# Performance work log

Measured on AMD Instinct MI355X. Metric: run time of the kernel, lower is better.

Reference implementation:

```python
import jax, jax.numpy as jnp
import numpy as np

NP, NA, E, DIN, DOUT = 50000, 50000, 800000, 128, 128


def setup_inputs() -> dict:
    key = jax.random.key(0)
    ks = jax.random.split(key, 16)
    inp = {
        'h_paper': jax.random.normal(ks[0], (NP, DIN), jnp.float32),
        'h_author': jax.random.normal(ks[1], (NA, DIN), jnp.float32),
        'W_r1': jax.random.normal(ks[2], (DIN, DOUT), jnp.float32) / np.sqrt(DIN),
        'W_r2': jax.random.normal(ks[3], (DIN, DOUT), jnp.float32) / np.sqrt(DIN),
        'W_r3': jax.random.normal(ks[4], (DIN, DOUT), jnp.float32) / np.sqrt(DIN),
        'att_W': jax.random.normal(ks[5], (DOUT, 128), jnp.float32) / np.sqrt(DOUT),
        'att_b': jax.random.normal(ks[6], (128,), jnp.float32) * 0.02,
        'att_q': jax.random.normal(ks[7], (128,), jnp.float32) / np.sqrt(128.0),
        'bn_gamma': jnp.ones((DOUT,), jnp.float32),
        'bn_beta': jnp.zeros((DOUT,), jnp.float32),
        'src_r1': jax.random.randint(ks[8], (E,), 0, NA, jnp.int32),
        'dst_r1': jax.random.randint(ks[9], (E,), 0, NP, jnp.int32),
        'src_r2': jax.random.randint(ks[10], (E,), 0, NP, jnp.int32),
        'dst_r2': jax.random.randint(ks[11], (E,), 0, NP, jnp.int32),
        'src_r3': jax.random.randint(ks[12], (E,), 0, NA, jnp.int32),
        'dst_r3': jax.random.randint(ks[13], (E,), 0, NA, jnp.int32),
    }
    return inp


def _graph_conv(h_src, W, src, dst, n_src, n_dst):
    # DGL GraphConv, norm='both', bias=False
    ones = jnp.ones(src.shape[0], h_src.dtype)
    deg_out = jnp.clip(jax.ops.segment_sum(ones, src, num_segments=n_src), 1.0)
    deg_in = jnp.clip(jax.ops.segment_sum(ones, dst, num_segments=n_dst), 1.0)
    m = (h_src * jax.lax.rsqrt(deg_out)[:, None]) @ W          # [n_src, Dout]
    agg = jax.ops.segment_sum(m[src], dst, num_segments=n_dst)  # [n_dst, Dout]
    return agg * jax.lax.rsqrt(deg_in)[:, None]


def _semantic_attention(z, att_W, att_b, att_q):
    # z: [R, N, D] per-relation outputs for one destination node type
    w = jnp.mean(jnp.tanh(z @ att_W + att_b) @ att_q, axis=1)  # [R]
    beta = jax.nn.softmax(w)
    return jnp.einsum('r,rnd->nd', beta, z)


def _post(x, gamma, beta):
    mu = jnp.mean(x, axis=0)
    var = jnp.var(x, axis=0)
    x = (x - mu) * jax.lax.rsqrt(var + 1e-5) * gamma + beta  # BatchNorm1d (train stats)
    return x * jax.lax.rsqrt(jnp.sum(x * x, axis=-1, keepdims=True) + 1e-12)  # L2 norm


def reference(h_paper, h_author, W_r1, W_r2, W_r3, att_W, att_b, att_q,
              bn_gamma, bn_beta, src_r1, dst_r1, src_r2, dst_r2, src_r3, dst_r3):
    n_p, n_a = h_paper.shape[0], h_author.shape[0]
    z_p1 = _graph_conv(h_author, W_r1, src_r1, dst_r1, n_a, n_p)  # author->paper
    z_p2 = _graph_conv(h_paper, W_r2, src_r2, dst_r2, n_p, n_p)   # paper->paper
    z_a1 = _graph_conv(h_author, W_r3, src_r3, dst_r3, n_a, n_a)  # author->author
    out_p = _semantic_attention(jnp.stack([z_p1, z_p2]), att_W, att_b, att_q)
    out_a = _semantic_attention(z_a1[None], att_W, att_b, att_q)
    out_p = _post(out_p, bn_gamma, bn_beta)
    out_a = _post(out_a, bn_gamma, bn_beta)
    return out_p, out_a
```

## Files before the change

kernel.cpp:

```cpp
#include <hip/hip_runtime.h>

#define DIM 128
#define NBLK 64
#define MAXTB 2560

static inline size_t align256(size_t x) { return (x + 255) & ~(size_t)255; }

__global__ void k_dout(const int* __restrict__ s1, int E1,
                       const int* __restrict__ s2, int E2,
                       const int* __restrict__ s3, int E3,
                       int* __restrict__ dout, int NM) {
  int i = blockIdx.x * blockDim.x + threadIdx.x;
  int st = gridDim.x * blockDim.x;
  int ET = E1 + E2 + E3;
  for (; i < ET; i += st) {
    const int* sp; int j, r;
    if (i < E1) { r = 0; j = i; sp = s1; }
    else if (i < E1 + E2) { r = 1; j = i - E1; sp = s2; }
    else { r = 2; j = i - E1 - E2; sp = s3; }
    atomicAdd(&dout[r * NM + sp[j]], 1);
  }
}

__global__ __launch_bounds__(256) void k_hist(const int* __restrict__ d1, int E1,
                                              const int* __restrict__ d2, int E2,
                                              const int* __restrict__ d3, int E3,
                                              int* __restrict__ Hmat, int NB, int TB) {
  __shared__ int hl[MAXTB];
  int t = threadIdx.x, b = blockIdx.x;
  for (int k = t; k < TB; k += 256) hl[k] = 0;
  __syncthreads();
  int ET = E1 + E2 + E3;
  int CH = (ET + NBLK - 1) / NBLK;
  int lo = b * CH, hi = min(lo + CH, ET);
  for (int i = lo + t; i < hi; i += 256) {
    const int* dp; int j, r;
    if (i < E1) { r = 0; j = i; dp = d1; }
    else if (i < E1 + E2) { r = 1; j = i - E1; dp = d2; }
    else { r = 2; j = i - E1 - E2; dp = d3; }
    int kb = r * NB + (dp[j] >> 6);
    atomicAdd(&hl[kb], 1);
  }
  __syncthreads();
  for (int k = t; k < TB; k += 256) Hmat[(size_t)k * NBLK + b] = hl[k];
}

__global__ __launch_bounds__(256) void k_scan1(const int* __restrict__ cnt,
                                               int* __restrict__ part, int M) {
  __shared__ int wsh[4];
  int t = threadIdx.x;
  int base = blockIdx.x * 2048 + t * 8;
  int s = 0;
  if (base + 8 <= M) {
    const int4* p = (const int4*)(cnt + base);
    int4 a = p[0], b = p[1];
    s = a.x + a.y + a.z + a.w + b.x + b.y + b.z + b.w;
  } else {
    for (int j = 0; j < 8; ++j) { int idx = base + j; if (idx < M) s += cnt[idx]; }
  }
#pragma unroll
  for (int off = 32; off; off >>= 1) s += __shfl_down(s, off, 64);
  int lane = t & 63, wid = t >> 6;
  if (lane == 0) wsh[wid] = s;
  __syncthreads();
  if (t == 0) part[blockIdx.x] = wsh[0] + wsh[1] + wsh[2] + wsh[3];
}

__global__ __launch_bounds__(256) void k_scan2(int* __restrict__ part, int B,
                                               int* __restrict__ rp, int M) {
  __shared__ int sh[256];
  int t = threadIdx.x;
  sh[t] = (t < B) ? part[t] : 0;
  __syncthreads();
  for (int off = 1; off < 256; off <<= 1) {
    int v = (t >= off) ? sh[t - off] : 0;
    __syncthreads();
    sh[t] += v;
    __syncthreads();
  }
  if (t < B) part[t] = t ? sh[t - 1] : 0;
  if (t == 0) rp[M] = sh[255];
}

__global__ __launch_bounds__(256) void k_scan3(const int* __restrict__ cnt,
                                               const int* __restrict__ part,
                                               int* __restrict__ rp, int M) {
  __shared__ int wsh[4];
  int t = threadIdx.x, lane = t & 63, wid = t >> 6;
  int base = blockIdx.x * 2048 + t * 8;
  int v[8];
  if (base + 8 <= M) {
    const int4* p = (const int4*)(cnt + base);
    int4 a = p[0], b = p[1];
    v[0] = a.x; v[1] = a.y; v[2] = a.z; v[3] = a.w;
    v[4] = b.x; v[5] = b.y; v[6] = b.z; v[7] = b.w;
  } else {
    for (int j = 0; j < 8; ++j) { int idx = base + j; v[j] = (idx < M) ? cnt[idx] : 0; }
  }
  int ts = 0;
#pragma unroll
  for (int j = 0; j < 8; ++j) ts += v[j];
  int incl = ts;
#pragma unroll
  for (int d = 1; d < 64; d <<= 1) { int u = __shfl_up(incl, d, 64); if (lane >= d) incl += u; }
  if (lane == 63) wsh[wid] = incl;
  __syncthreads();
  int woff = 0;
  for (int w = 0; w < wid; ++w) woff += wsh[w];
  int run = part[blockIdx.x] + woff + incl - ts;
#pragma unroll
  for (int j = 0; j < 8; ++j) {
    int idx = base + j;
    if (idx < M) rp[idx] = run;
    run += v[j];
  }
}

__global__ __launch_bounds__(256) void k_scatter(const int* __restrict__ s1, const int* __restrict__ d1, int E1,
                                                 const int* __restrict__ s2, const int* __restrict__ d2, int E2,
                                                 const int* __restrict__ s3, const int* __restrict__ d3, int E3,
                                                 const int* __restrict__ rp,
                                                 unsigned* __restrict__ ebuf, int NB, int TB) {
  __shared__ int curl[MAXTB];
  int t = threadIdx.x, b = blockIdx.x;
  for (int k = t; k < TB; k += 256) curl[k] = rp[(size_t)k * NBLK + b];
  __syncthreads();
  int ET = E1 + E2 + E3;
  int CH = (ET + NBLK - 1) / NBLK;
  int lo = b * CH, hi = min(lo + CH, ET);
  for (int i = lo + t; i < hi; i += 256) {
    const int* sp; const int* dp; int j, r;
    if (i < E1) { r = 0; j = i; sp = s1; dp = d1; }
    else if (i < E1 + E2) { r = 1; j = i - E1; sp = s2; dp = d2; }
    else { r = 2; j = i - E1 - E2; sp = s3; dp = d3; }
    int dst = dp[j];
    int kb = r * NB + (dst >> 6);
    int pos = atomicAdd(&curl[kb], 1);
    ebuf[pos] = ((unsigned)(dst & 63) << 16) | (unsigned)sp[j];
  }
}

__global__ __launch_bounds__(256) void k_bsort(const unsigned* __restrict__ ebuf,
                                               const int* __restrict__ rp,
                                               unsigned short* __restrict__ ebuf2,
                                               int* __restrict__ rp2, int* __restrict__ deg,
                                               int NB, int NM) {
  __shared__ int hist[64];
  __shared__ int cursor[64];
  int t = threadIdx.x;
  int k = blockIdx.x;
  if (t < 64) hist[t] = 0;
  __syncthreads();
  int start = rp[(size_t)k * NBLK];
  int end = rp[(size_t)(k + 1) * NBLK];
  for (int e = start + t; e < end; e += 256)
    atomicAdd(&hist[ebuf[e] >> 16], 1);
  __syncthreads();
  if (t < 64) {
    int v = hist[t];
    int incl = v;
#pragma unroll
    for (int d = 1; d < 64; d <<= 1) { int u = __shfl_up(incl, d, 64); if (t >= d) incl += u; }
    int excl = incl - v;
    cursor[t] = start + excl;
    int r = k / NB, bb = k - r * NB;
    int ld = bb * 64 + t;
    if (ld < NM) {
      rp2[r * NM + ld] = start + excl;
      deg[r * NM + ld] = v;
    }
  }
  __syncthreads();
  for (int e = start + t; e < end; e += 256) {
    unsigned p = ebuf[e];
    int pos = atomicAdd(&cursor[p >> 16], 1);
    ebuf2[pos] = (unsigned short)(p & 0xFFFF);
  }
}

__global__ __launch_bounds__(256) void k_pull2(const float* __restrict__ m,
                                               const int* __restrict__ rp2,
                                               const int* __restrict__ deg,
                                               const unsigned short* __restrict__ ebuf2,
                                               float* __restrict__ z, int N) {
  int lane = threadIdx.x & 63, wid = threadIdx.x >> 6;
  int gw = blockIdx.x * 4 + wid, nw = gridDim.x * 4;
  for (int n = gw; n < N; n += nw) {
    int b = rp2[n], d = deg[n];
    float ax = 0.f, ay = 0.f;
    for (int e = b; e < b + d; ++e) {
      int s = ebuf2[e];
      float2 v = *(const float2*)(m + (size_t)s * DIM + 2 * lane);
      ax += v.x; ay += v.y;
    }
    float sc = rsqrtf(fmaxf((float)d, 1.0f));
    float2 o; o.x = ax * sc; o.y = ay * sc;
    *(float2*)(z + (size_t)n * DIM + 2 * lane) = o;
  }
}

__global__ __launch_bounds__(512) void k_gemm(const float* __restrict__ h,
                                              const float* __restrict__ W,
                                              const int* __restrict__ degout,
                                              float* __restrict__ m, int N) {
  __shared__ float Wl[DIM * DIM];
  for (int i = threadIdx.x; i < DIM * DIM; i += 512) Wl[i] = W[i];
  __syncthreads();
  int lane = threadIdx.x & 63, wid = threadIdx.x >> 6;
  int gw = blockIdx.x * 8 + wid, nw = gridDim.x * 8;
  for (int n = gw; n < N; n += nw) {
    float s = rsqrtf(fmaxf((float)degout[n], 1.0f));
    const float4* h4 = (const float4*)(h + (size_t)n * DIM);
    float ax = 0.f, ay = 0.f;
#pragma unroll 4
    for (int k4 = 0; k4 < 32; ++k4) {
      float4 hv = h4[k4];
      int k = k4 * 4;
      float2 w0 = *(const float2*)&Wl[(k + 0) * DIM + 2 * lane];
      float2 w1 = *(const float2*)&Wl[(k + 1) * DIM + 2 * lane];
      float2 w2 = *(const float2*)&Wl[(k + 2) * DIM + 2 * lane];
      float2 w3 = *(const float2*)&Wl[(k + 3) * DIM + 2 * lane];
      ax = fmaf(hv.x, w0.x, ax); ay = fmaf(hv.x, w0.y, ay);
      ax = fmaf(hv.y, w1.x, ax); ay = fmaf(hv.y, w1.y, ay);
      ax = fmaf(hv.z, w2.x, ax); ay = fmaf(hv.z, w2.y, ay);
      ax = fmaf(hv.w, w3.x, ax); ay = fmaf(hv.w, w3.y, ay);
    }
    float2 o; o.x = s * ax; o.y = s * ay;
    *(float2*)(m + (size_t)n * DIM + 2 * lane) = o;
  }
}

__global__ __launch_bounds__(512) void k_att(const float* __restrict__ z1,
                                             const float* __restrict__ z2,
                                             const float* __restrict__ attW,
                                             const float* __restrict__ attb,
                                             const float* __restrict__ attq,
                                             float* __restrict__ wsum, int N) {
  __shared__ float Wl[DIM * DIM];
  for (int i = threadIdx.x; i < DIM * DIM; i += 512) Wl[i] = attW[i];
  int lane = threadIdx.x & 63, wid = threadIdx.x >> 6;
  float b0 = attb[2 * lane], b1 = attb[2 * lane + 1];
  float q0 = attq[2 * lane], q1 = attq[2 * lane + 1];
  __syncthreads();
  int gw = blockIdx.x * 8 + wid, nw = gridDim.x * 8;
  float a1 = 0.f, a2 = 0.f;
  for (int n = gw; n < N; n += nw) {
    const float4* p1 = (const float4*)(z1 + (size_t)n * DIM);
    const float4* p2 = (const float4*)(z2 + (size_t)n * DIM);
    float c1x = 0, c1y = 0, c2x = 0, c2y = 0;
#pragma unroll 4
    for (int k4 = 0; k4 < 32; ++k4) {
      float4 u = p1[k4];
      float4 v = p2[k4];
      int k = k4 * 4;
      float2 w0 = *(const float2*)&Wl[(k + 0) * DIM + 2 * lane];
      float2 w1 = *(const float2*)&Wl[(k + 1) * DIM + 2 * lane];
      float2 w2 = *(const float2*)&Wl[(k + 2) * DIM + 2 * lane];
      float2 w3 = *(const float2*)&Wl[(k + 3) * DIM + 2 * lane];
      c1x = fmaf(u.x, w0.x, c1x); c1y = fmaf(u.x, w0.y, c1y);
      c2x = fmaf(v.x, w0.x, c2x); c2y = fmaf(v.x, w0.y, c2y);
      c1x = fmaf(u.y, w1.x, c1x); c1y = fmaf(u.y, w1.y, c1y);
      c2x = fmaf(v.y, w1.x, c2x); c2y = fmaf(v.y, w1.y, c2y);
      c1x = fmaf(u.z, w2.x, c1x); c1y = fmaf(u.z, w2.y, c1y);
      c2x = fmaf(v.z, w2.x, c2x); c2y = fmaf(v.z, w2.y, c2y);
      c1x = fmaf(u.w, w3.x, c1x); c1y = fmaf(u.w, w3.y, c1y);
      c2x = fmaf(v.w, w3.x, c2x); c2y = fmaf(v.w, w3.y, c2y);
    }
    a1 += tanhf(c1x + b0) * q0 + tanhf(c1y + b1) * q1;
    a2 += tanhf(c2x + b0) * q0 + tanhf(c2y + b1) * q1;
  }
#pragma unroll
  for (int off = 32; off; off >>= 1) {
    a1 += __shfl_down(a1, off, 64);
    a2 += __shfl_down(a2, off, 64);
  }
  __syncthreads();
  if (lane == 0) { Wl[wid] = a1; Wl[8 + wid] = a2; }
  __syncthreads();
  if (threadIdx.x == 0) {
    float s1 = 0, s2 = 0;
    for (int w = 0; w < 8; ++w) { s1 += Wl[w]; s2 += Wl[8 + w]; }
    atomicAdd(&wsum[0], s1);
    atomicAdd(&wsum[1], s2);
  }
}

__global__ void k_combine(float* __restrict__ x, const float* __restrict__ z2,
                          const float* __restrict__ wsum, float invN, int total4) {
  float w1 = wsum[0] * invN, w2 = wsum[1] * invN;
  float mx = fmaxf(w1, w2);
  float e1 = expf(w1 - mx), e2 = expf(w2 - mx);
  float inv = 1.f / (e1 + e2);
  float b1 = e1 * inv, b2 = e2 * inv;
  float4* x4 = (float4*)x;
  const float4* z4 = (const float4*)z2;
  int i = blockIdx.x * blockDim.x + threadIdx.x;
  int st = gridDim.x * blockDim.x;
  for (; i < total4; i += st) {
    float4 a = x4[i], b = z4[i];
    a.x = b1 * a.x + b2 * b.x;
    a.y = b1 * a.y + b2 * b.y;
    a.z = b1 * a.z + b2 * b.z;
    a.w = b1 * a.w + b2 * b.w;
    x4[i] = a;
  }
}

__global__ __launch_bounds__(128) void k_stats2(const float* __restrict__ xp,
                                                const float* __restrict__ xa,
                                                int NP, int NA, float* __restrict__ st) {
  int d = threadIdx.x;
  float sp = 0, qp = 0, sa = 0, qa = 0;
  for (int n = blockIdx.x; n < NP; n += gridDim.x) {
    float v = xp[(size_t)n * DIM + d]; sp += v; qp += v * v;
  }
  for (int n = blockIdx.x; n < NA; n += gridDim.x) {
    float v = xa[(size_t)n * DIM + d]; sa += v; qa += v * v;
  }
  atomicAdd(&st[d], sp);
  atomicAdd(&st[DIM + d], qp);
  atomicAdd(&st[2 * DIM + d], sa);
  atomicAdd(&st[3 * DIM + d], qa);
}

__global__ __launch_bounds__(256) void k_post2(float* __restrict__ xp, float* __restrict__ xa,
                                               const float* __restrict__ st,
                                               const float* __restrict__ gamma,
                                               const float* __restrict__ beta,
                                               int NP, int NA) {
  int lane = threadIdx.x & 63;
  int wv = blockIdx.x * 4 + (threadIdx.x >> 6), nw = gridDim.x * 4;
  int d0 = 2 * lane, d1 = d0 + 1;
  {
    float invN = 1.f / (float)NP;
    float mu0 = st[d0] * invN, mu1 = st[d1] * invN;
    float g0 = gamma[d0] * rsqrtf(st[DIM + d0] * invN - mu0 * mu0 + 1e-5f);
    float g1 = gamma[d1] * rsqrtf(st[DIM + d1] * invN - mu1 * mu1 + 1e-5f);
    float b0 = beta[d0], b1 = beta[d1];
    for (int n = wv; n < NP; n += nw) {
      float2 v = *(float2*)(xp + (size_t)n * DIM + d0);
      float y0 = fmaf(v.x - mu0, g0, b0);
      float y1 = fmaf(v.y - mu1, g1, b1);
      float p = y0 * y0 + y1 * y1;
#pragma unroll
      for (int off = 32; off; off >>= 1) p += __shfl_xor(p, off, 64);
      float r = rsqrtf(p + 1e-12f);
      float2 o; o.x = y0 * r; o.y = y1 * r;
      *(float2*)(xp + (size_t)n * DIM + d0) = o;
    }
  }
  {
    float invN = 1.f / (float)NA;
    float mu0 = st[2 * DIM + d0] * invN, mu1 = st[2 * DIM + d1] * invN;
    float g0 = gamma[d0] * rsqrtf(st[3 * DIM + d0] * invN - mu0 * mu0 + 1e-5f);
    float g1 = gamma[d1] * rsqrtf(st[3 * DIM + d1] * invN - mu1 * mu1 + 1e-5f);
    float b0 = beta[d0], b1 = beta[d1];
    for (int n = wv; n < NA; n += nw) {
      float2 v = *(float2*)(xa + (size_t)n * DIM + d0);
      float y0 = fmaf(v.x - mu0, g0, b0);
      float y1 = fmaf(v.y - mu1, g1, b1);
      float p = y0 * y0 + y1 * y1;
#pragma unroll
      for (int off = 32; off; off >>= 1) p += __shfl_xor(p, off, 64);
      float r = rsqrtf(p + 1e-12f);
      float2 o; o.x = y0 * r; o.y = y1 * r;
      *(float2*)(xa + (size_t)n * DIM + d0) = o;
    }
  }
}

extern "C" void kernel_launch(void* const* d_in, const int* in_sizes, int n_in,
                              void* d_out, int out_size, void* d_ws, size_t ws_size,
                              hipStream_t stream) {
  const float* h_paper  = (const float*)d_in[0];
  const float* h_author = (const float*)d_in[1];
  const float* W_r1 = (const float*)d_in[2];
  const float* W_r2 = (const float*)d_in[3];
  const float* W_r3 = (const float*)d_in[4];
  const float* att_W = (const float*)d_in[5];
  const float* att_b = (const float*)d_in[6];
  const float* att_q = (const float*)d_in[7];
  const float* bn_g = (const float*)d_in[8];
  const float* bn_b = (const float*)d_in[9];
  const int* src_r1 = (const int*)d_in[10];
  const int* dst_r1 = (const int*)d_in[11];
  const int* src_r2 = (const int*)d_in[12];
  const int* dst_r2 = (const int*)d_in[13];
  const int* src_r3 = (const int*)d_in[14];
  const int* dst_r3 = (const int*)d_in[15];

  int NP = in_sizes[0] / DIM;
  int NA = in_sizes[1] / DIM;
  int E1 = in_sizes[10], E2 = in_sizes[12], E3 = in_sizes[14];
  int ET = E1 + E2 + E3;
  int NM = NP > NA ? NP : NA;
  int NB = (NM + 63) >> 6;
  int TB = 3 * NB;
  int M = TB * NBLK;
  int B = (M + 2047) / 2048;

  char* ws = (char*)d_ws;
  size_t off = 0;
  float* m_buf = (float*)(ws + off);    off += align256((size_t)NM * DIM * 4);
  float* z2    = (float*)(ws + off);    off += align256((size_t)NP * DIM * 4);
  unsigned* ebuf = (unsigned*)(ws + off); off += align256((size_t)ET * 4);
  unsigned short* ebuf2 = (unsigned short*)(ws + off); off += align256((size_t)ET * 2);
  int* Hmat    = (int*)(ws + off);      off += align256((size_t)M * 4);
  int* rp      = (int*)(ws + off);      off += align256(((size_t)M + 1) * 4);
  int* rp2     = (int*)(ws + off);      off += align256((size_t)3 * NM * 4);
  int* deg     = (int*)(ws + off);      off += align256((size_t)3 * NM * 4);
  int* part    = (int*)(ws + off);      off += align256(256 * 4);
  size_t zoff = off;
  int* dout    = (int*)(ws + off);      off += (size_t)3 * NM * 4;
  float* wsum  = (float*)(ws + off);    off += 2 * 4;
  float* stats = (float*)(ws + off);    off += 4 * DIM * 4;
  size_t zbytes = off - zoff;

  float* xp = (float*)d_out;
  float* xa = (float*)d_out + (size_t)NP * DIM;

  hipMemsetAsync(ws + zoff, 0, zbytes, stream);

  k_dout<<<2048, 256, 0, stream>>>(src_r1, E1, src_r2, E2, src_r3, E3, dout, NM);

  k_hist<<<NBLK, 256, 0, stream>>>(dst_r1, E1, dst_r2, E2, dst_r3, E3, Hmat, NB, TB);
  k_scan1<<<B, 256, 0, stream>>>(Hmat, part, M);
  k_scan2<<<1, 256, 0, stream>>>(part, B, rp, M);
  k_scan3<<<B, 256, 0, stream>>>(Hmat, part, rp, M);
  k_scatter<<<NBLK, 256, 0, stream>>>(src_r1, dst_r1, E1, src_r2, dst_r2, E2,
                                      src_r3, dst_r3, E3, rp, ebuf, NB, TB);
  k_bsort<<<TB, 256, 0, stream>>>(ebuf, rp, ebuf2, rp2, deg, NB, NM);

  k_gemm<<<512, 512, 0, stream>>>(h_author, W_r1, dout, m_buf, NA);
  k_pull2<<<2048, 256, 0, stream>>>(m_buf, rp2, deg, ebuf2, xp, NP);
  k_gemm<<<512, 512, 0, stream>>>(h_paper, W_r2, dout + NM, m_buf, NP);
  k_pull2<<<2048, 256, 0, stream>>>(m_buf, rp2 + NM, deg + NM, ebuf2, z2, NP);
  k_gemm<<<512, 512, 0, stream>>>(h_author, W_r3, dout + 2 * NM, m_buf, NA);
  k_pull2<<<2048, 256, 0, stream>>>(m_buf, rp2 + 2 * NM, deg + 2 * NM, ebuf2, xa, NA);

  k_att<<<512, 512, 0, stream>>>(xp, z2, att_W, att_b, att_q, wsum, NP);
  k_combine<<<2048, 256, 0, stream>>>(xp, z2, wsum, 1.0f / (float)NP, NP * DIM / 4);

  k_stats2<<<1024, 128, 0, stream>>>(xp, xa, NP, NA, stats);
  k_post2<<<2048, 256, 0, stream>>>(xp, xa, stats, bn_g, bn_b, NP, NA);
}
```

Baseline: 1.015 ms.

## Register-block GEMM and attention over four nodes, split pull wavefront into halves

The GEMM and attention kernels now process four nodes per wavefront, so each LDS weight fragment is reused across four rows instead of one. This cuts LDS traffic per FMA and raises instruction-level parallelism. The pull kernel gives each half-wavefront its own destination node and uses float4 gathers, doubling the number of nodes handled at once. The cost is more register pressure and possible divergence between half-waves that have different degrees.

Result: faster. 993.4 us (-2.1%).

```diff
diff --git a/kernel.cpp b/kernel.cpp
--- a/kernel.cpp
+++ b/kernel.cpp
@@ -184,18 +184,24 @@
                                                const unsigned short* __restrict__ ebuf2,
                                                float* __restrict__ z, int N) {
   int lane = threadIdx.x & 63, wid = threadIdx.x >> 6;
+  int half = lane >> 5, hl = lane & 31;
   int gw = blockIdx.x * 4 + wid, nw = gridDim.x * 4;
-  for (int n = gw; n < N; n += nw) {
-    int b = rp2[n], d = deg[n];
-    float ax = 0.f, ay = 0.f;
-    for (int e = b; e < b + d; ++e) {
-      int s = ebuf2[e];
-      float2 v = *(const float2*)(m + (size_t)s * DIM + 2 * lane);
-      ax += v.x; ay += v.y;
-    }
-    float sc = rsqrtf(fmaxf((float)d, 1.0f));
-    float2 o; o.x = ax * sc; o.y = ay * sc;
-    *(float2*)(z + (size_t)n * DIM + 2 * lane) = o;
+  for (int n0 = gw * 2; n0 < N; n0 += nw * 2) {
+    int n = n0 + half;
+    bool valid = n < N;
+    int b = 0, d = 0;
+    if (valid) { b = rp2[n]; d = deg[n]; }
+    float ax = 0.f, ay = 0.f, az = 0.f, aw = 0.f;
+    for (int i = 0; i < d; ++i) {
+      int s = ebuf2[b + i];
+      float4 v = *(const float4*)(m + (size_t)s * DIM + hl * 4);
+      ax += v.x; ay += v.y; az += v.z; aw += v.w;
+    }
+    if (valid) {
+      float sc = rsqrtf(fmaxf((float)d, 1.0f));
+      float4 o; o.x = ax * sc; o.y = ay * sc; o.z = az * sc; o.w = aw * sc;
+      *(float4*)(z + (size_t)n * DIM + hl * 4) = o;
+    }
   }
 }
 
@@ -208,25 +214,56 @@
   __syncthreads();
   int lane = threadIdx.x & 63, wid = threadIdx.x >> 6;
   int gw = blockIdx.x * 8 + wid, nw = gridDim.x * 8;
-  for (int n = gw; n < N; n += nw) {
-    float s = rsqrtf(fmaxf((float)degout[n], 1.0f));
-    const float4* h4 = (const float4*)(h + (size_t)n * DIM);
-    float ax = 0.f, ay = 0.f;
-#pragma unroll 4
+  for (int n0 = gw * 4; n0 < N; n0 += nw * 4) {
+    int nc1 = min(n0 + 1, N - 1), nc2 = min(n0 + 2, N - 1), nc3 = min(n0 + 3, N - 1);
+    const float4* h0 = (const float4*)(h + (size_t)n0 * DIM);
+    const float4* h1 = (const float4*)(h + (size_t)nc1 * DIM);
+    const float4* h2 = (const float4*)(h + (size_t)nc2 * DIM);
+    const float4* h3 = (const float4*)(h + (size_t)nc3 * DIM);
+    float ax0 = 0, ay0 = 0, ax1 = 0, ay1 = 0, ax2 = 0, ay2 = 0, ax3 = 0, ay3 = 0;
+#pragma unroll 2
     for (int k4 = 0; k4 < 32; ++k4) {
-      float4 hv = h4[k4];
+      float4 u0 = h0[k4], u1 = h1[k4], u2 = h2[k4], u3 = h3[k4];
       int k = k4 * 4;
       float2 w0 = *(const float2*)&Wl[(k + 0) * DIM + 2 * lane];
       float2 w1 = *(const float2*)&Wl[(k + 1) * DIM + 2 * lane];
       float2 w2 = *(const float2*)&Wl[(k + 2) * DIM + 2 * lane];
       float2 w3 = *(const float2*)&Wl[(k + 3) * DIM + 2 * lane];
-      ax = fmaf(hv.x, w0.x, ax); ay = fmaf(hv.x, w0.y, ay);
-      ax = fmaf(hv.y, w1.x, ax); ay = fmaf(hv.y, w1.y, ay);
-      ax = fmaf(hv.z, w2.x, ax); ay = fmaf(hv.z, w2.y, ay);
-      ax = fmaf(hv.w, w3.x, ax); ay = fmaf(hv.w, w3.y, ay);
-    }
-    float2 o; o.x = s * ax; o.y = s * ay;
-    *(float2*)(m + (size_t)n * DIM + 2 * lane) = o;
+      ax0 = fmaf(u0.x, w0.x, ax0); ay0 = fmaf(u0.x, w0.y, ay0);
+      ax1 = fmaf(u1.x, w0.x, ax1); ay1 = fmaf(u1.x, w0.y, ay1);
+      ax2 = fmaf(u2.x, w0.x, ax2); ay2 = fmaf(u2.x, w0.y, ay2);
+      ax3 = fmaf(u3.x, w0.x, ax3); ay3 = fmaf(u3.x, w0.y, ay3);
+      ax0 = fmaf(u0.y, w1.x, ax0); ay0 = fmaf(u0.y, w1.y, ay0);
+      ax1 = fmaf(u1.y, w1.x, ax1); ay1 = fmaf(u1.y, w1.y, ay1);
+      ax2 = fmaf(u2.y, w1.x, ax2); ay2 = fmaf(u2.y, w1.y, ay2);
+      ax3 = fmaf(u3.y, w1.x, ax3); ay3 = fmaf(u3.y, w1.y, ay3);
+      ax0 = fmaf(u0.z, w2.x, ax0); ay0 = fmaf(u0.z, w2.y, ay0);
+      ax1 = fmaf(u1.z, w2.x, ax1); ay1 = fmaf(u1.z, w2.y, ay1);
+      ax2 = fmaf(u2.z, w2.x, ax2); ay2 = fmaf(u2.z, w2.y, ay2);
+      ax3 = fmaf(u3.z, w2.x, ax3); ay3 = fmaf(u3.z, w2.y, ay3);
+      ax0 = fmaf(u0.w, w3.x, ax0); ay0 = fmaf(u0.w, w3.y, ay0);
+      ax1 = fmaf(u1.w, w3.x, ax1); ay1 = fmaf(u1.w, w3.y, ay1);
+      ax2 = fmaf(u2.w, w3.x, ax2); ay2 = fmaf(u2.w, w3.y, ay2);
+      ax3 = fmaf(u3.w, w3.x, ax3); ay3 = fmaf(u3.w, w3.y, ay3);
+    }
+    float s0 = rsqrtf(fmaxf((float)degout[n0], 1.0f));
+    float2 o0; o0.x = s0 * ax0; o0.y = s0 * ay0;
+    *(float2*)(m + (size_t)n0 * DIM + 2 * lane) = o0;
+    if (n0 + 1 < N) {
+      float s = rsqrtf(fmaxf((float)degout[n0 + 1], 1.0f));
+      float2 o; o.x = s * ax1; o.y = s * ay1;
+      *(float2*)(m + (size_t)(n0 + 1) * DIM + 2 * lane) = o;
+    }
+    if (n0 + 2 < N) {
+      float s = rsqrtf(fmaxf((float)degout[n0 + 2], 1.0f));
+      float2 o; o.x = s * ax2; o.y = s * ay2;
+      *(float2*)(m + (size_t)(n0 + 2) * DIM + 2 * lane) = o;
+    }
+    if (n0 + 3 < N) {
+      float s = rsqrtf(fmaxf((float)degout[n0 + 3], 1.0f));
+      float2 o; o.x = s * ax3; o.y = s * ay3;
+      *(float2*)(m + (size_t)(n0 + 3) * DIM + 2 * lane) = o;
+    }
   }
 }
 
@@ -244,30 +281,68 @@
   __syncthreads();
   int gw = blockIdx.x * 8 + wid, nw = gridDim.x * 8;
   float a1 = 0.f, a2 = 0.f;
-  for (int n = gw; n < N; n += nw) {
-    const float4* p1 = (const float4*)(z1 + (size_t)n * DIM);
-    const float4* p2 = (const float4*)(z2 + (size_t)n * DIM);
-    float c1x = 0, c1y = 0, c2x = 0, c2y = 0;
-#pragma unroll 4
+  for (int n0 = gw * 4; n0 < N; n0 += nw * 4) {
+    int nc1 = min(n0 + 1, N - 1), nc2 = min(n0 + 2, N - 1), nc3 = min(n0 + 3, N - 1);
+    const float4* p0 = (const float4*)(z1 + (size_t)n0 * DIM);
+    const float4* p1 = (const float4*)(z1 + (size_t)nc1 * DIM);
+    const float4* p2 = (const float4*)(z1 + (size_t)nc2 * DIM);
+    const float4* p3 = (const float4*)(z1 + (size_t)nc3 * DIM);
+    const float4* r0 = (const float4*)(z2 + (size_t)n0 * DIM);
+    const float4* r1 = (const float4*)(z2 + (size_t)nc1 * DIM);
+    const float4* r2 = (const float4*)(z2 + (size_t)nc2 * DIM);
+    const float4* r3 = (const float4*)(z2 + (size_t)nc3 * DIM);
+    float cx[4] = {0, 0, 0, 0}, cy[4] = {0, 0, 0, 0};
+    float dx[4] = {0, 0, 0, 0}, dy[4] = {0, 0, 0, 0};
+#pragma unroll 2
     for (int k4 = 0; k4 < 32; ++k4) {
-      float4 u = p1[k4];
-      float4 v = p2[k4];
+      float4 u0 = p0[k4], u1 = p1[k4], u2 = p2[k4], u3 = p3[k4];
+      float4 v0 = r0[k4], v1 = r1[k4], v2 = r2[k4], v3 = r3[k4];
       int k = k4 * 4;
       float2 w0 = *(const float2*)&Wl[(k + 0) * DIM + 2 * lane];
       float2 w1 = *(const float2*)&Wl[(k + 1) * DIM + 2 * lane];
       float2 w2 = *(const float2*)&Wl[(k + 2) * DIM + 2 * lane];
       float2 w3 = *(const float2*)&Wl[(k + 3) * DIM + 2 * lane];
-      c1x = fmaf(u.x, w0.x, c1x); c1y = fmaf(u.x, w0.y, c1y);
-      c2x = fmaf(v.x, w0.x, c2x); c2y = fmaf(v.x, w0.y, c2y);
-      c1x = fmaf(u.y, w1.x, c1x); c1y = fmaf(u.y, w1.y, c1y);
-      c2x = fmaf(v.y, w1.x, c2x); c2y = fmaf(v.y, w1.y, c2y);
-      c1x = fmaf(u.z, w2.x, c1x); c1y = fmaf(u.z, w2.y, c1y);
-      c2x = fmaf(v.z, w2.x, c2x); c2y = fmaf(v.z, w2.y, c2y);
-      c1x = fmaf(u.w, w3.x, c1x); c1y = fmaf(u.w, w3.y, c1y);
-      c2x = fmaf(v.w, w3.x, c2x); c2y = fmaf(v.w, w3.y, c2y);
-    }
-    a1 += tanhf(c1x + b0) * q0 + tanhf(c1y + b1) * q1;
-    a2 += tanhf(c2x + b0) * q0 + tanhf(c2y + b1) * q1;
+      cx[0] = fmaf(u0.x, w0.x, cx[0]); cy[0] = fmaf(u0.x, w0.y, cy[0]);
+      cx[1] = fmaf(u1.x, w0.x, cx[1]); cy[1] = fmaf(u1.x, w0.y, cy[1]);
+      cx[2] = fmaf(u2.x, w0.x, cx[2]); cy[2] = fmaf(u2.x, w0.y, cy[2]);
+      cx[3] = fmaf(u3.x, w0.x, cx[3]); cy[3] = fmaf(u3.x, w0.y, cy[3]);
+      dx[0] = fmaf(v0.x, w0.x, dx[0]); dy[0] = fmaf(v0.x, w0.y, dy[0]);
+      dx[1] = fmaf(v1.x, w0.x, dx[1]); dy[1] = fmaf(v1.x, w0.y, dy[1]);
+      dx[2] = fmaf(v2.x, w0.x, dx[2]); dy[2] = fmaf(v2.x, w0.y, dy[2]);
+      dx[3] = fmaf(v3.x, w0.x, dx[3]); dy[3] = fmaf(v3.x, w0.y, dy[3]);
+      cx[0] = fmaf(u0.y, w1.x, cx[0]); cy[0] = fmaf(u0.y, w1.y, cy[0]);
+      cx[1] = fmaf(u1.y, w1.x, cx[1]); cy[1] = fmaf(u1.y, w1.y, cy[1]);
+      cx[2] = fmaf(u2.y, w1.x, cx[2]); cy[2] = fmaf(u2.y, w1.y, cy[2]);
+      cx[3] = fmaf(u3.y, w1.x, cx[3]); cy[3] = fmaf(u3.y, w1.y, cy[3]);
+      dx[0] = fmaf(v0.y, w1.x, dx[0]); dy[0] = fmaf(v0.y, w1.y, dy[0]);
+      dx[1] = fmaf(v1.y, w1.x, dx[1]); dy[1] = fmaf(v1.y, w1.y, dy[1]);
+      dx[2] = fmaf(v2.y, w1.x, dx[2]); dy[2] = fmaf(v2.y, w1.y, dy[2]);
+      dx[3] = fmaf(v3.y, w1.x, dx[3]); dy[3] = fmaf(v3.y, w1.y, dy[3]);
+      cx[0] = fmaf(u0.z, w2.x, cx[0]); cy[0] = fmaf(u0.z, w2.y, cy[0]);
+      cx[1] = fmaf(u1.z, w2.x, cx[1]); cy[1] = fmaf(u1.z, w2.y, cy[1]);
+      cx[2] = fmaf(u2.z, w2.x, cx[2]); cy[2] = fmaf(u2.z, w2.y, cy[2]);
+      cx[3] = fmaf(u3.z, w2.x, cx[3]); cy[3] = fmaf(u3.z, w2.y, cy[3]);
+      dx[0] = fmaf(v0.z, w2.x, dx[0]); dy[0] = fmaf(v0.z, w2.y, dy[0]);
+      dx[1] = fmaf(v1.z, w2.x, dx[1]); dy[1] = fmaf(v1.z, w2.y, dy[1]);
+      dx[2] = fmaf(v2.z, w2.x, dx[2]); dy[2] = fmaf(v2.z, w2.y, dy[2]);
+      dx[3] = fmaf(v3.z, w2.x, dx[3]); dy[3] = fmaf(v3.z, w2.y, dy[3]);
+      cx[0] = fmaf(u0.w, w3.x, cx[0]); cy[0] = fmaf(u0.w, w3.y, cy[0]);
+      cx[1] = fmaf(u1.w, w3.x, cx[1]); cy[1] = fmaf(u1.w, w3.y, cy[1]);
+      cx[2] = fmaf(u2.w, w3.x, cx[2]); cy[2] = fmaf(u2.w, w3.y, cy[2]);
+      cx[3] = fmaf(u3.w, w3.x, cx[3]); cy[3] = fmaf(u3.w, w3.y, cy[3]);
+      dx[0] = fmaf(v0.w, w3.x, dx[0]); dy[0] = fmaf(v0.w, w3.y, dy[0]);
+      dx[1] = fmaf(v1.w, w3.x, dx[1]); dy[1] = fmaf(v1.w, w3.y, dy[1]);
+      dx[2] = fmaf(v2.w, w3.x, dx[2]); dy[2] = fmaf(v2.w, w3.y, dy[2]);
+      dx[3] = fmaf(v3.w, w3.x, dx[3]); dy[3] = fmaf(v3.w, w3.y, dy[3]);
+    }
+    int nv = N - n0;
+#pragma unroll
+    for (int j = 0; j < 4; ++j) {
+      if (j < nv) {
+        a1 += tanhf(cx[j] + b0) * q0 + tanhf(cy[j] + b1) * q1;
+        a2 += tanhf(dx[j] + b0) * q0 + tanhf(dy[j] + b1) * q1;
+      }
+    }
   }
 #pragma unroll
   for (int off = 32; off; off >>= 1) {
```

## Store GraphConv messages as bf16, register-block GEMM, fuse combine with BN stats

Applied to the files above, without the earlier changes.

The GEMM now computes four nodes per wave so each shared-memory weight load is reused four times, and it writes the message matrix as packed bf16, halving its size. The pull kernel gathers bf16 rows with half a wave per destination node, two nodes per wave, and unrolls edges by two. The attention combine and the batch-norm statistics pass become one kernel with shared-memory reductions, removing a kernel launch and one read of the paper output. In exchange, messages lose precision from bf16 rounding, which may push results past the tolerance.

After: 923.5 us. 1.1x faster.

```diff
diff --git a/kernel.cpp b/kernel.cpp
--- a/kernel.cpp
+++ b/kernel.cpp
@@ -5,6 +5,14 @@
 #define MAXTB 2560
 
 static inline size_t align256(size_t x) { return (x + 255) & ~(size_t)255; }
+
+__device__ __forceinline__ unsigned pack2_bf16(float a, float b) {
+  unsigned ua = __float_as_uint(a);
+  unsigned ub = __float_as_uint(b);
+  ua += 0x7FFFu + ((ua >> 16) & 1u);
+  ub += 0x7FFFu + ((ub >> 16) & 1u);
+  return (ua >> 16) | (ub & 0xFFFF0000u);
+}
 
 __global__ void k_dout(const int* __restrict__ s1, int E1,
                        const int* __restrict__ s2, int E2,
@@ -178,55 +186,100 @@
   }
 }
 
-__global__ __launch_bounds__(256) void k_pull2(const float* __restrict__ m,
+__global__ __launch_bounds__(256) void k_pull2(const uint2* __restrict__ mv,
                                                const int* __restrict__ rp2,
                                                const int* __restrict__ deg,
                                                const unsigned short* __restrict__ ebuf2,
                                                float* __restrict__ z, int N) {
   int lane = threadIdx.x & 63, wid = threadIdx.x >> 6;
+  int half = lane >> 5, hl = lane & 31;
   int gw = blockIdx.x * 4 + wid, nw = gridDim.x * 4;
-  for (int n = gw; n < N; n += nw) {
-    int b = rp2[n], d = deg[n];
-    float ax = 0.f, ay = 0.f;
-    for (int e = b; e < b + d; ++e) {
-      int s = ebuf2[e];
-      float2 v = *(const float2*)(m + (size_t)s * DIM + 2 * lane);
-      ax += v.x; ay += v.y;
-    }
-    float sc = rsqrtf(fmaxf((float)d, 1.0f));
-    float2 o; o.x = ax * sc; o.y = ay * sc;
-    *(float2*)(z + (size_t)n * DIM + 2 * lane) = o;
+  for (int n0 = gw * 2; n0 < N; n0 += nw * 2) {
+    int n = n0 + half;
+    bool valid = n < N;
+    int b = 0, d = 0;
+    if (valid) { b = rp2[n]; d = deg[n]; }
+    float ax = 0.f, ay = 0.f, az = 0.f, aw = 0.f;
+    int i = 0;
+    for (; i + 2 <= d; i += 2) {
+      int s0 = ebuf2[b + i];
+      int s1 = ebuf2[b + i + 1];
+      uint2 v0 = mv[(size_t)s0 * 32 + hl];
+      uint2 v1 = mv[(size_t)s1 * 32 + hl];
+      ax += __uint_as_float(v0.x << 16); ay += __uint_as_float(v0.x & 0xFFFF0000u);
+      az += __uint_as_float(v0.y << 16); aw += __uint_as_float(v0.y & 0xFFFF0000u);
+      ax += __uint_as_float(v1.x << 16); ay += __uint_as_float(v1.x & 0xFFFF0000u);
+      az += __uint_as_float(v1.y << 16); aw += __uint_as_float(v1.y & 0xFFFF0000u);
+    }
+    if (i < d) {
+      int s0 = ebuf2[b + i];
+      uint2 v0 = mv[(size_t)s0 * 32 + hl];
+      ax += __uint_as_float(v0.x << 16); ay += __uint_as_float(v0.x & 0xFFFF0000u);
+      az += __uint_as_float(v0.y << 16); aw += __uint_as_float(v0.y & 0xFFFF0000u);
+    }
+    if (valid) {
+      float sc = rsqrtf(fmaxf((float)d, 1.0f));
+      float4 o; o.x = ax * sc; o.y = ay * sc; o.z = az * sc; o.w = aw * sc;
+      *(float4*)(z + (size_t)n * DIM + hl * 4) = o;
+    }
   }
 }
 
 __global__ __launch_bounds__(512) void k_gemm(const float* __restrict__ h,
                                               const float* __restrict__ W,
                                               const int* __restrict__ degout,
-                                              float* __restrict__ m, int N) {
+                                              unsigned* __restrict__ m16, int N) {
   __shared__ float Wl[DIM * DIM];
   for (int i = threadIdx.x; i < DIM * DIM; i += 512) Wl[i] = W[i];
   __syncthreads();
   int lane = threadIdx.x & 63, wid = threadIdx.x >> 6;
   int gw = blockIdx.x * 8 + wid, nw = gridDim.x * 8;
-  for (int n = gw; n < N; n += nw) {
-    float s = rsqrtf(fmaxf((float)degout[n], 1.0f));
-    const float4* h4 = (const float4*)(h + (size_t)n * DIM);
-    float ax = 0.f, ay = 0.f;
-#pragma unroll 4
+  for (int n0 = gw * 4; n0 < N; n0 += nw * 4) {
+    int nc1 = min(n0 + 1, N - 1), nc2 = min(n0 + 2, N - 1), nc3 = min(n0 + 3, N - 1);
+    const float4* h0 = (const float4*)(h + (size_t)n0 * DIM);
+    const float4* h1 = (const float4*)(h + (size_t)nc1 * DIM);
+    const float4* h2 = (const float4*)(h + (size_t)nc2 * DIM);
+    const float4* h3 = (const float4*)(h + (size_t)nc3 * DIM);
+    float ax0 = 0, ay0 = 0, ax1 = 0, ay1 = 0, ax2 = 0, ay2 = 0, ax3 = 0, ay3 = 0;
+#pragma unroll 2
     for (int k4 = 0; k4 < 32; ++k4) {
-      float4 hv = h4[k4];
+      float4 u0 = h0[k4], u1 = h1[k4], u2 = h2[k4], u3 = h3[k4];
       int k = k4 * 4;
       float2 w0 = *(const float2*)&Wl[(k + 0) * DIM + 2 * lane];
       float2 w1 = *(const float2*)&Wl[(k + 1) * DIM + 2 * lane];
       float2 w2 = *(const float2*)&Wl[(k + 2) * DIM + 2 * lane];
       float2 w3 = *(const float2*)&Wl[(k + 3) * DIM + 2 * lane];
-      ax = fmaf(hv.x, w0.x, ax); ay = fmaf(hv.x, w0.y, ay);
-      ax = fmaf(hv.y, w1.x, ax); ay = fmaf(hv.y, w1.y, ay);
-      ax = fmaf(hv.z, w2.x, ax); ay = fmaf(hv.z, w2.y, ay);
-      ax = fmaf(hv.w, w3.x, ax); ay = fmaf(hv.w, w3.y, ay);
-    }
-    float2 o; o.x = s * ax; o.y = s * ay;
-    *(float2*)(m + (size_t)n * DIM + 2 * lane) = o;
+      ax0 = fmaf(u0.x, w0.x, ax0); ay0 = fmaf(u0.x, w0.y, ay0);
+      ax1 = fmaf(u1.x, w0.x, ax1); ay1 = fmaf(u1.x, w0.y, ay1);
+      ax2 = fmaf(u2.x, w0.x, ax2); ay2 = fmaf(u2.x, w0.y, ay2);
+      ax3 = fmaf(u3.x, w0.x, ax3); ay3 = fmaf(u3.x, w0.y, ay3);
+      ax0 = fmaf(u0.y, w1.x, ax0); ay0 = fmaf(u0.y, w1.y, ay0);
+      ax1 = fmaf(u1.y, w1.x, ax1); ay1 = fmaf(u1.y, w1.y, ay1);
+      ax2 = fmaf(u2.y, w1.x, ax2); ay2 = fmaf(u2.y, w1.y, ay2);
+      ax3 = fmaf(u3.y, w1.x, ax3); ay3 = fmaf(u3.y, w1.y, ay3);
+      ax0 = fmaf(u0.z, w2.x, ax0); ay0 = fmaf(u0.z, w2.y, ay0);
+      ax1 = fmaf(u1.z, w2.x, ax1); ay1 = fmaf(u1.z, w2.y, ay1);
+      ax2 = fmaf(u2.z, w2.x, ax2); ay2 = fmaf(u2.z, w2.y, ay2);
+      ax3 = fmaf(u3.z, w2.x, ax3); ay3 = fmaf(u3.z, w2.y, ay3);
+      ax0 = fmaf(u0.w, w3.x, ax0); ay0 = fmaf(u0.w, w3.y, ay0);
+      ax1 = fmaf(u1.w, w3.x, ax1); ay1 = fmaf(u1.w, w3.y, ay1);
+      ax2 = fmaf(u2.w, w3.x, ax2); ay2 = fmaf(u2.w, w3.y, ay2);
+      ax3 = fmaf(u3.w, w3.x, ax3); ay3 = fmaf(u3.w, w3.y, ay3);
+    }
+    float s0 = rsqrtf(fmaxf((float)degout[n0], 1.0f));
+    m16[(size_t)n0 * 64 + lane] = pack2_bf16(s0 * ax0, s0 * ay0);
+    if (n0 + 1 < N) {
+      float s = rsqrtf(fmaxf((float)degout[n0 + 1], 1.0f));
+      m16[(size_t)(n0 + 1) * 64 + lane] = pack2_bf16(s * ax1, s * ay1);
+    }
+    if (n0 + 2 < N) {
+      float s = rsqrtf(fmaxf((float)degout[n0 + 2], 1.0f));
+      m16[(size_t)(n0 + 2) * 64 + lane] = pack2_bf16(s * ax2, s * ay2);
+    }
+    if (n0 + 3 < N) {
+      float s = rsqrtf(fmaxf((float)degout[n0 + 3], 1.0f));
+      m16[(size_t)(n0 + 3) * 64 + lane] = pack2_bf16(s * ax3, s * ay3);
+    }
   }
 }
 
@@ -285,42 +338,89 @@
   }
 }
 
-__global__ void k_combine(float* __restrict__ x, const float* __restrict__ z2,
-                          const float* __restrict__ wsum, float invN, int total4) {
-  float w1 = wsum[0] * invN, w2 = wsum[1] * invN;
+__global__ __launch_bounds__(256) void k_comb_stats(float* __restrict__ xp,
+                                                    const float* __restrict__ z2,
+                                                    const float* __restrict__ xa,
+                                                    const float* __restrict__ wsum,
+                                                    float invNP, int np4, int na4,
+                                                    float* __restrict__ st) {
+  float w1 = wsum[0] * invNP, w2 = wsum[1] * invNP;
   float mx = fmaxf(w1, w2);
   float e1 = expf(w1 - mx), e2 = expf(w2 - mx);
   float inv = 1.f / (e1 + e2);
   float b1 = e1 * inv, b2 = e2 * inv;
-  float4* x4 = (float4*)x;
+  int t = threadIdx.x;
+  int i0 = blockIdx.x * 256 + t;
+  int stride = gridDim.x * 256;
+  float4* x4 = (float4*)xp;
   const float4* z4 = (const float4*)z2;
-  int i = blockIdx.x * blockDim.x + threadIdx.x;
-  int st = gridDim.x * blockDim.x;
-  for (; i < total4; i += st) {
+  const float4* a4 = (const float4*)xa;
+  float s0 = 0, s1 = 0, s2 = 0, s3 = 0, q0 = 0, q1 = 0, q2 = 0, q3 = 0;
+  for (int i = i0; i < np4; i += stride) {
     float4 a = x4[i], b = z4[i];
     a.x = b1 * a.x + b2 * b.x;
     a.y = b1 * a.y + b2 * b.y;
     a.z = b1 * a.z + b2 * b.z;
     a.w = b1 * a.w + b2 * b.w;
     x4[i] = a;
-  }
-}
-
-__global__ __launch_bounds__(128) void k_stats2(const float* __restrict__ xp,
-                                                const float* __restrict__ xa,
-                                                int NP, int NA, float* __restrict__ st) {
-  int d = threadIdx.x;
-  float sp = 0, qp = 0, sa = 0, qa = 0;
-  for (int n = blockIdx.x; n < NP; n += gridDim.x) {
-    float v = xp[(size_t)n * DIM + d]; sp += v; qp += v * v;
-  }
-  for (int n = blockIdx.x; n < NA; n += gridDim.x) {
-    float v = xa[(size_t)n * DIM + d]; sa += v; qa += v * v;
-  }
-  atomicAdd(&st[d], sp);
-  atomicAdd(&st[DIM + d], qp);
-  atomicAdd(&st[2 * DIM + d], sa);
-  atomicAdd(&st[3 * DIM + d], qa);
+    s0 += a.x; s1 += a.y; s2 += a.z; s3 += a.w;
+    q0 += a.x * a.x; q1 += a.y * a.y; q2 += a.z * a.z; q3 += a.w * a.w;
+  }
+  __shared__ float red[256 * 4];
+  int c = t & 31;
+  red[t * 4 + 0] = s0; red[t * 4 + 1] = s1; red[t * 4 + 2] = s2; red[t * 4 + 3] = s3;
+  __syncthreads();
+  if (t < 32) {
+    float r0 = 0, r1 = 0, r2 = 0, r3 = 0;
+    for (int j = 0; j < 8; ++j) {
+      int tt = t + 32 * j;
+      r0 += red[tt * 4 + 0]; r1 += red[tt * 4 + 1]; r2 += red[tt * 4 + 2]; r3 += red[tt * 4 + 3];
+    }
+    atomicAdd(&st[4 * t + 0], r0); atomicAdd(&st[4 * t + 1], r1);
+    atomicAdd(&st[4 * t + 2], r2); atomicAdd(&st[4 * t + 3], r3);
+  }
+  __syncthreads();
+  red[t * 4 + 0] = q0; red[t * 4 + 1] = q1; red[t * 4 + 2] = q2; red[t * 4 + 3] = q3;
+  __syncthreads();
+  if (t < 32) {
+    float r0 = 0, r1 = 0, r2 = 0, r3 = 0;
+    for (int j = 0; j < 8; ++j) {
+      int tt = t + 32 * j;
+      r0 += red[tt * 4 + 0]; r1 += red[tt * 4 + 1]; r2 += red[tt * 4 + 2]; r3 += red[tt * 4 + 3];
+    }
+    atomicAdd(&st[DIM + 4 * t + 0], r0); atomicAdd(&st[DIM + 4 * t + 1], r1);
+    atomicAdd(&st[DIM + 4 * t + 2], r2); atomicAdd(&st[DIM + 4 * t + 3], r3);
+  }
+  __syncthreads();
+  s0 = s1 = s2 = s3 = q0 = q1 = q2 = q3 = 0;
+  for (int i = i0; i < na4; i += stride) {
+    float4 a = a4[i];
+    s0 += a.x; s1 += a.y; s2 += a.z; s3 += a.w;
+    q0 += a.x * a.x; q1 += a.y * a.y; q2 += a.z * a.z; q3 += a.w * a.w;
+  }
+  red[t * 4 + 0] = s0; red[t * 4 + 1] = s1; red[t * 4 + 2] = s2; red[t * 4 + 3] = s3;
+  __syncthreads();
+  if (t < 32) {
+    float r0 = 0, r1 = 0, r2 = 0, r3 = 0;
+    for (int j = 0; j < 8; ++j) {
+      int tt = t + 32 * j;
+      r0 += red[tt * 4 + 0]; r1 += red[tt * 4 + 1]; r2 += red[tt * 4 + 2]; r3 += red[tt * 4 + 3];
+    }
+    atomicAdd(&st[2 * DIM + 4 * t + 0], r0); atomicAdd(&st[2 * DIM + 4 * t + 1], r1);
+    atomicAdd(&st[2 * DIM + 4 * t + 2], r2); atomicAdd(&st[2 * DIM + 4 * t + 3], r3);
+  }
+  __syncthreads();
+  red[t * 4 + 0] = q0; red[t * 4 + 1] = q1; red[t * 4 + 2] = q2; red[t * 4 + 3] = q3;
+  __syncthreads();
+  if (t < 32) {
+    float r0 = 0, r1 = 0, r2 = 0, r3 = 0;
+    for (int j = 0; j < 8; ++j) {
+      int tt = t + 32 * j;
+      r0 += red[tt * 4 + 0]; r1 += red[tt * 4 + 1]; r2 += red[tt * 4 + 2]; r3 += red[tt * 4 + 3];
+    }
+    atomicAdd(&st[3 * DIM + 4 * t + 0], r0); atomicAdd(&st[3 * DIM + 4 * t + 1], r1);
+    atomicAdd(&st[3 * DIM + 4 * t + 2], r2); atomicAdd(&st[3 * DIM + 4 * t + 3], r3);
+  }
 }
 
 __global__ __launch_bounds__(256) void k_post2(float* __restrict__ xp, float* __restrict__ xa,
@@ -401,7 +501,7 @@
 
   char* ws = (char*)d_ws;
   size_t off = 0;
-  float* m_buf = (float*)(ws + off);    off += align256((size_t)NM * DIM * 4);
+  unsigned* m16 = (unsigned*)(ws + off); off += align256((size_t)NM * 64 * 4);
   float* z2    = (float*)(ws + off);    off += align256((size_t)NP * DIM * 4);
   unsigned* ebuf = (unsigned*)(ws + off); off += align256((size_t)ET * 4);
   unsigned short* ebuf2 = (unsigned short*)(ws + off); off += align256((size_t)ET * 2);
@@ -431,16 +531,17 @@
                                       src_r3, dst_r3, E3, rp, ebuf, NB, TB);
   k_bsort<<<TB, 256, 0, stream>>>(ebuf, rp, ebuf2, rp2, deg, NB, NM);
 
-  k_gemm<<<512, 512, 0, stream>>>(h_author, W_r1, dout, m_buf, NA);
-  k_pull2<<<2048, 256, 0, stream>>>(m_buf, rp2, deg, ebuf2, xp, NP);
-  k_gemm<<<512, 512, 0, stream>>>(h_paper, W_r2, dout + NM, m_buf, NP);
-  k_pull2<<<2048, 256, 0, stream>>>(m_buf, rp2 + NM, deg + NM, ebuf2, z2, NP);
-  k_gemm<<<512, 512, 0, stream>>>(h_author, W_r3, dout + 2 * NM, m_buf, NA);
-  k_pull2<<<2048, 256, 0, stream>>>(m_buf, rp2 + 2 * NM, deg + 2 * NM, ebuf2, xa, NA);
+  const uint2* mv = (const uint2*)m16;
+  k_gemm<<<512, 512, 0, stream>>>(h_author, W_r1, dout, m16, NA);
+  k_pull2<<<2048, 256, 0, stream>>>(mv, rp2, deg, ebuf2, xp, NP);
+  k_gemm<<<512, 512, 0, stream>>>(h_paper, W_r2, dout + NM, m16, NP);
+  k_pull2<<<2048, 256, 0, stream>>>(mv, rp2 + NM, deg + NM, ebuf2, z2, NP);
+  k_gemm<<<512, 512, 0, stream>>>(h_author, W_r3, dout + 2 * NM, m16, NA);
+  k_pull2<<<2048, 256, 0, stream>>>(mv, rp2 + 2 * NM, deg + 2 * NM, ebuf2, xa, NA);
 
   k_att<<<512, 512, 0, stream>>>(xp, z2, att_W, att_b, att_q, wsum, NP);
-  k_combine<<<2048, 256, 0, stream>>>(xp, z2, wsum, 1.0f / (float)NP, NP * DIM / 4);
-
-  k_stats2<<<1024, 128, 0, stream>>>(xp, xa, NP, NA, stats);
+  k_comb_stats<<<512, 256, 0, stream>>>(xp, z2, xa, wsum, 1.0f / (float)NP,
+                                        NP * DIM / 4, NA * DIM / 4, stats);
+
   k_post2<<<2048, 256, 0, stream>>>(xp, xa, stats, bn_g, bn_b, NP, NA);
 }
```
